# Optimization experiments

Hardware: AMD Instinct MI355X
Metric: run time of the kernel (lower is better)

The kernel has to match this reference:

```python
import jax, jax.numpy as jnp
import numpy as np

NUM_GROUPS = 32
NUM_HEADS = 4
EPS = 1e-5


def setup_inputs() -> dict:
    key = jax.random.key(0)
    ks = jax.random.split(key, 6)
    B, C, H, W = 16, 512, 32, 32
    x = jax.random.normal(ks[0], (B, C, H, W), dtype=jnp.float32)
    gn_w = jax.random.normal(ks[1], (C,), dtype=jnp.float32) * 0.02 + 1.0
    gn_b = jax.random.normal(ks[2], (C,), dtype=jnp.float32) * 0.02
    # 1x1 convs are channel matmuls: store as [out_ch, in_ch]
    w_qkv = jax.random.normal(ks[3], (3 * C, C), dtype=jnp.float32) * (C ** -0.5)
    w_out = jax.random.normal(ks[4], (C, C), dtype=jnp.float32) * (C ** -0.5)
    b_out = jax.random.normal(ks[5], (C,), dtype=jnp.float32) * 0.02
    return {"x": x, "gn_w": gn_w, "gn_b": gn_b, "w_qkv": w_qkv, "w_out": w_out, "b_out": b_out}


def _group_norm(x, w, b):
    B, C, H, W = x.shape
    g = NUM_GROUPS
    xg = x.reshape(B, g, C // g, H, W)
    mean = xg.mean(axis=(2, 3, 4), keepdims=True)
    var = xg.var(axis=(2, 3, 4), keepdims=True)
    xn = ((xg - mean) * jax.lax.rsqrt(var + EPS)).reshape(B, C, H, W)
    return xn * w[None, :, None, None] + b[None, :, None, None]


def reference(x, gn_w, gn_b, w_qkv, w_out, b_out):
    B, C, H, W = x.shape
    h = NUM_HEADS
    d = C // h
    scale = d ** -0.5
    xn = _group_norm(x, gn_w, gn_b)
    # 1x1 conv QKV projection: [3C, C] @ channels
    qkv = jnp.einsum('oc,bchw->bohw', w_qkv, xn)
    q, k, v = jnp.split(qkv, 3, axis=1)
    # [B, h, d, HW]
    q = q.reshape(B, h, d, H * W)
    k = k.reshape(B, h, d, H * W)
    v = v.reshape(B, h, d, H * W)
    scores = jnp.einsum('bhdi,bhdj->bhij', q, k) * scale
    probs = jax.nn.softmax(scores, axis=-1)
    out = jnp.einsum('bhij,bhdj->bhdi', probs, v)
    out = out.reshape(B, C, H, W)
    out = jnp.einsum('oc,bchw->bohw', w_out, out) + b_out[None, :, None, None]
    return out + x
```

## Files before the change

kernel.cpp:

```cpp
#include <hip/hip_runtime.h>
#include <hip/hip_bf16.h>

#define B_    16
#define C_    512
#define HW_   1024
#define G_    32
#define CPG_  16
#define NH_   4
#define D_    128
#define EPS_  1e-5f
#define SCALE_ 0.08838834764831845f
#define SCALE_L2E_ 0.1275174306f

typedef short bf16x8 __attribute__((ext_vector_type(8)));
typedef short bf16x4 __attribute__((ext_vector_type(4)));
typedef float f32x4  __attribute__((ext_vector_type(4)));

typedef __attribute__((address_space(3))) unsigned int lds_u32_t;
typedef const __attribute__((address_space(1))) unsigned int glb_u32_t;

__device__ __forceinline__ bf16x8 ld8(const __hip_bfloat16* p) {
    return *reinterpret_cast<const bf16x8*>(p);
}
__device__ __forceinline__ void gload16(const __hip_bfloat16* g, __hip_bfloat16* l) {
    __builtin_amdgcn_global_load_lds((glb_u32_t*)(const void*)g,
                                     (lds_u32_t*)(void*)l, 16, 0, 0);
}
__device__ __forceinline__ unsigned pack_bf2(float a, float b) {
    union { __hip_bfloat16 h; unsigned short u; } ua, ub;
    ua.h = __float2bfloat16(a); ub.h = __float2bfloat16(b);
    return ((unsigned)ub.u << 16) | (unsigned)ua.u;
}

__global__ __launch_bounds__(256) void convert_w(
    const float* __restrict__ wqkv, const float* __restrict__ wout,
    __hip_bfloat16* __restrict__ wqkv_bf, __hip_bfloat16* __restrict__ wout_bf) {
    const int i = (blockIdx.x * 256 + threadIdx.x) * 4;
    if (i < 3 * C_ * C_) {
        float4 v = *reinterpret_cast<const float4*>(wqkv + i);
        union { bf16x4 s; __hip_bfloat16 h[4]; } u;
        u.h[0] = __float2bfloat16(v.x); u.h[1] = __float2bfloat16(v.y);
        u.h[2] = __float2bfloat16(v.z); u.h[3] = __float2bfloat16(v.w);
        *reinterpret_cast<bf16x4*>(wqkv_bf + i) = u.s;
    }
    if (i < C_ * C_) {
        float4 v = *reinterpret_cast<const float4*>(wout + i);
        union { bf16x4 s; __hip_bfloat16 h[4]; } u;
        u.h[0] = __float2bfloat16(v.x); u.h[1] = __float2bfloat16(v.y);
        u.h[2] = __float2bfloat16(v.z); u.h[3] = __float2bfloat16(v.w);
        *reinterpret_cast<bf16x4*>(wout_bf + i) = u.s;
    }
}

__global__ __launch_bounds__(256) void gn_kernel(
    const float* __restrict__ x, const float* __restrict__ gnw,
    const float* __restrict__ gnb, __hip_bfloat16* __restrict__ xn_t) {
    const int b = blockIdx.x >> 5;
    const int g = blockIdx.x & 31;
    const float* xp = x + ((size_t)(b * C_ + g * CPG_)) * HW_;

    float s = 0.f, s2 = 0.f;
    const float4* xv = reinterpret_cast<const float4*>(xp);
    #pragma unroll
    for (int t = 0; t < 16; ++t) {
        float4 v = xv[threadIdx.x + t * 256];
        s  += v.x + v.y + v.z + v.w;
        s2 += v.x * v.x + v.y * v.y + v.z * v.z + v.w * v.w;
    }
    #pragma unroll
    for (int off = 32; off > 0; off >>= 1) {
        s  += __shfl_down(s,  off, 64);
        s2 += __shfl_down(s2, off, 64);
    }
    __shared__ float ss[4], ss2[4];
    if ((threadIdx.x & 63) == 0) { ss[threadIdx.x >> 6] = s; ss2[threadIdx.x >> 6] = s2; }
    __syncthreads();
    s = ss[0] + ss[1] + ss[2] + ss[3];
    s2 = ss2[0] + ss2[1] + ss2[2] + ss2[3];
    const float mean = s * (1.f / 16384.f);
    const float inv  = rsqrtf(fmaxf(s2 * (1.f / 16384.f) - mean * mean, 0.f) + EPS_);

    float a[16], bb[16];
    #pragma unroll
    for (int cc = 0; cc < 16; ++cc) {
        float w = gnw[g * CPG_ + cc];
        a[cc] = inv * w;
        bb[cc] = gnb[g * CPG_ + cc] - mean * inv * w;
    }

    for (int hw = threadIdx.x; hw < HW_; hw += 256) {
        union { bf16x8 v; __hip_bfloat16 h[8]; } u0, u1;
        #pragma unroll
        for (int cc = 0; cc < 8; ++cc)
            u0.h[cc] = __float2bfloat16(xp[cc * HW_ + hw] * a[cc] + bb[cc]);
        #pragma unroll
        for (int cc = 8; cc < 16; ++cc)
            u1.h[cc - 8] = __float2bfloat16(xp[cc * HW_ + hw] * a[cc] + bb[cc]);
        __hip_bfloat16* dst = xn_t + ((size_t)(b * HW_ + hw)) * C_ + g * CPG_;
        *reinterpret_cast<bf16x8*>(dst) = u0.v;
        *reinterpret_cast<bf16x8*>(dst + 8) = u1.v;
    }
}

#define PH_(r, s) (((r) * 8 + ((s) ^ ((r) & 7))) * 8)

__global__ __launch_bounds__(256, 3) void qkv_gemm(
    const __hip_bfloat16* __restrict__ W, const __hip_bfloat16* __restrict__ xn_t,
    __hip_bfloat16* __restrict__ q_t, __hip_bfloat16* __restrict__ k_t,
    __hip_bfloat16* __restrict__ v_s) {
    const int id   = blockIdx.x;
    const int virt = (id & 7) * 192 + (id >> 3);
    const int ot   = virt % 12;
    const int rest = virt / 12;
    const int itl  = rest & 7;
    const int b    = rest >> 3;
    const int o0 = ot * 128, i0 = itl * 128;

    const int t = threadIdx.x;
    const int w = t >> 6, lane = t & 63, l16 = lane & 15, lg = lane >> 4;
    const int wr = w >> 1, wc = w & 1;
    const __hip_bfloat16* xb = xn_t + (size_t)b * HW_ * C_;

    __shared__ __align__(16) __hip_bfloat16 Ab[128 * 64];
    __shared__ __align__(16) __hip_bfloat16 Bb[128 * 64];

    const int r8  = lane >> 3;
    const int ssl = (lane & 7) ^ r8;
    auto issue = [&](int kk) {
        #pragma unroll
        for (int j = 0; j < 4; ++j) {
            const int row = w * 32 + j * 8 + r8;
            gload16(W  + (size_t)(o0 + row) * C_ + kk + ssl * 8, &Ab[(w * 32 + j * 8) * 64]);
            gload16(xb + (size_t)(i0 + row) * C_ + kk + ssl * 8, &Bb[(w * 32 + j * 8) * 64]);
        }
    };

    f32x4 acc[4][4];
    const f32x4 z = {0.f, 0.f, 0.f, 0.f};
    #pragma unroll
    for (int m = 0; m < 4; ++m)
        #pragma unroll
        for (int n = 0; n < 4; ++n) acc[m][n] = z;

    for (int ks = 0; ks < 8; ++ks) {
        issue(ks * 64);
        __syncthreads();
        #pragma unroll
        for (int kks = 0; kks < 2; ++kks) {
            bf16x8 af[4], bfr[4];
            #pragma unroll
            for (int m = 0; m < 4; ++m)
                af[m] = ld8(&Ab[PH_(wr * 64 + m * 16 + l16, kks * 4 + lg)]);
            #pragma unroll
            for (int n = 0; n < 4; ++n)
                bfr[n] = ld8(&Bb[PH_(wc * 64 + n * 16 + l16, kks * 4 + lg)]);
            if (ot < 8) {
                #pragma unroll
                for (int m = 0; m < 4; ++m)
                    #pragma unroll
                    for (int n = 0; n < 4; ++n)
                        acc[m][n] = __builtin_amdgcn_mfma_f32_16x16x32_bf16(bfr[n], af[m], acc[m][n], 0, 0, 0);
            } else {
                #pragma unroll
                for (int m = 0; m < 4; ++m)
                    #pragma unroll
                    for (int n = 0; n < 4; ++n)
                        acc[m][n] = __builtin_amdgcn_mfma_f32_16x16x32_bf16(af[m], bfr[n], acc[m][n], 0, 0, 0);
            }
        }
        if (ks < 7) __syncthreads();
    }

    if (ot < 4) {
        const int hd = ot;
        __hip_bfloat16* base = q_t + (size_t)(b * NH_ + hd) * HW_ * D_;
        const int dd = wr * 64 + l16;
        #pragma unroll
        for (int m = 0; m < 4; ++m)
            #pragma unroll
            for (int n = 0; n < 4; ++n)
                #pragma unroll
                for (int r = 0; r < 4; ++r) {
                    const int i = i0 + wc * 64 + n * 16 + lg * 4 + r;
                    base[(size_t)i * D_ + dd + m * 16] = __float2bfloat16(acc[m][n][r] * SCALE_L2E_);
                }
    } else if (ot < 8) {
        const int hd = ot - 4;
        __hip_bfloat16* base = k_t + (size_t)(b * NH_ + hd) * HW_ * D_;
        const int dd = wr * 64 + l16;
        #pragma unroll
        for (int m = 0; m < 4; ++m)
            #pragma unroll
            for (int n = 0; n < 4; ++n)
                #pragma unroll
                for (int r = 0; r < 4; ++r) {
                    const int i = i0 + wc * 64 + n * 16 + lg * 4 + r;
                    base[(size_t)i * D_ + dd + m * 16] = __float2bfloat16(acc[m][n][r]);
                }
    } else {
        const int hd = ot - 8;
        __hip_bfloat16* base = v_s + (size_t)(b * NH_ + hd) * D_ * HW_;
        #pragma unroll
        for (int m = 0; m < 4; ++m)
            #pragma unroll
            for (int r = 0; r < 4; ++r) {
                const int dd = wr * 64 + m * 16 + lg * 4 + r;
                #pragma unroll
                for (int n = 0; n < 4; ++n) {
                    const int i = i0 + wc * 64 + n * 16 + l16;
                    base[(size_t)dd * HW_ + i] = __float2bfloat16(acc[m][n][r]);
                }
            }
    }
}

__global__ __launch_bounds__(512, 4) void attn_kernel(
    const __hip_bfloat16* __restrict__ q_t, const __hip_bfloat16* __restrict__ k_t,
    const __hip_bfloat16* __restrict__ v_s, __hip_bfloat16* __restrict__ at) {
    const int id  = blockIdx.x;
    const int xcd = id & 7;
    const int q8  = id >> 3;
    const int hb  = xcd * 8 + (q8 >> 3);
    const int it  = q8 & 7;
    const int h   = hb & 3;
    const int b   = hb >> 2;

    const int t = threadIdx.x;
    const int w  = t >> 6;
    const int lane = t & 63;
    const int l16 = lane & 15, lg = lane >> 4;
    const size_t bh = (size_t)b * NH_ + h;
    const __hip_bfloat16* qp = q_t + bh * HW_ * D_;
    const __hip_bfloat16* kp = k_t + bh * HW_ * D_;
    const __hip_bfloat16* vp = v_s + bh * D_ * HW_;
    const int i0 = it * 128 + w * 16;

    __shared__ __align__(16) __hip_bfloat16 kbuf[64 * 128];
    __shared__ __align__(16) __hip_bfloat16 vbuf[128 * 64];
    __shared__ __align__(16) __hip_bfloat16 P2[8][16][72];

    #define KPHYS(row, c) (((row) * 16 + ((c) ^ ((row) & 7))) * 8)
    #define VPHYS(row, c) (((row) * 8  + ((c) ^ ((row) & 7))) * 8)

    const int krow = t >> 3, kc = t & 7;
    const int vrow = t >> 2, vc = t & 3;

    bf16x8 kreg0, kreg1, vreg0, vreg1;
    auto issue_loads = [&](int j0) {
        kreg0 = ld8(kp + (size_t)(j0 + krow) * D_ + kc * 8);
        kreg1 = ld8(kp + (size_t)(j0 + krow) * D_ + (kc + 8) * 8);
        vreg0 = ld8(vp + (size_t)vrow * HW_ + j0 + vc * 8);
        vreg1 = ld8(vp + (size_t)vrow * HW_ + j0 + (vc + 4) * 8);
    };

    bf16x8 aq[4];
    #pragma unroll
    for (int kd = 0; kd < 4; ++kd)
        aq[kd] = ld8(qp + (size_t)(i0 + l16) * D_ + kd * 32 + lg * 8);

    f32x4 accO[8];
    const f32x4 z = {0.f, 0.f, 0.f, 0.f};
    #pragma unroll
    for (int tt = 0; tt < 8; ++tt) accO[tt] = z;
    float m_run = -INFINITY;
    float l_run = 0.f;

    issue_loads(0);

    for (int jb = 0; jb < 16; ++jb) {
        __syncthreads();
        *reinterpret_cast<bf16x8*>(&kbuf[KPHYS(krow, kc)])     = kreg0;
        *reinterpret_cast<bf16x8*>(&kbuf[KPHYS(krow, kc + 8)]) = kreg1;
        *reinterpret_cast<bf16x8*>(&vbuf[VPHYS(vrow, vc)])     = vreg0;
        *reinterpret_cast<bf16x8*>(&vbuf[VPHYS(vrow, vc + 4)]) = vreg1;
        __syncthreads();
        if (jb < 15) issue_loads((jb + 1) * 64);

        f32x4 st[4];
        #pragma unroll
        for (int jt = 0; jt < 4; ++jt) st[jt] = z;
        #pragma unroll
        for (int jt = 0; jt < 4; ++jt)
            #pragma unroll
            for (int kd = 0; kd < 4; ++kd) {
                bf16x8 bk = ld8(&kbuf[KPHYS(jt * 16 + l16, kd * 4 + lg)]);
                st[jt] = __builtin_amdgcn_mfma_f32_16x16x32_bf16(bk, aq[kd], st[jt], 0, 0, 0);
            }

        float mx = fmaxf(fmaxf(st[0][0], st[0][1]), fmaxf(st[0][2], st[0][3]));
        #pragma unroll
        for (int jt = 1; jt < 4; ++jt)
            mx = fmaxf(mx, fmaxf(fmaxf(st[jt][0], st[jt][1]), fmaxf(st[jt][2], st[jt][3])));
        mx = fmaxf(mx, __shfl_xor(mx, 16, 64));
        mx = fmaxf(mx, __shfl_xor(mx, 32, 64));

        if (__any(mx > m_run + 8.f)) {
            float mnew = fmaxf(m_run, mx);
            float alpha = exp2f(m_run - mnew);
            m_run = mnew;
            l_run *= alpha;
            float al[4];
            #pragma unroll
            for (int r = 0; r < 4; ++r) al[r] = __shfl(alpha, lg * 4 + r, 64);
            const f32x4 a4 = {al[0], al[1], al[2], al[3]};
            #pragma unroll
            for (int tt = 0; tt < 8; ++tt) accO[tt] *= a4;
        }

        float sum = 0.f;
        #pragma unroll
        for (int jt = 0; jt < 4; ++jt) {
            float p0 = exp2f(st[jt][0] - m_run), p1 = exp2f(st[jt][1] - m_run);
            float p2 = exp2f(st[jt][2] - m_run), p3 = exp2f(st[jt][3] - m_run);
            sum += (p0 + p1) + (p2 + p3);
            uint2 uu = { pack_bf2(p0, p1), pack_bf2(p2, p3) };
            *reinterpret_cast<uint2*>(&P2[w][l16][jt * 16 + lg * 4]) = uu;
        }
        sum += __shfl_xor(sum, 16, 64);
        sum += __shfl_xor(sum, 32, 64);
        l_run += sum;

        #pragma unroll
        for (int ks = 0; ks < 2; ++ks) {
            bf16x8 pa = ld8(&P2[w][l16][ks * 32 + lg * 8]);
            #pragma unroll
            for (int dt = 0; dt < 8; ++dt) {
                bf16x8 bv = ld8(&vbuf[VPHYS(dt * 16 + l16, ks * 4 + lg)]);
                accO[dt] = __builtin_amdgcn_mfma_f32_16x16x32_bf16(pa, bv, accO[dt], 0, 0, 0);
            }
        }
    }

    const float linv = 1.f / l_run;
    float rl[4];
    #pragma unroll
    for (int r = 0; r < 4; ++r) rl[r] = __shfl(linv, lg * 4 + r, 64);
    #pragma unroll
    for (int r = 0; r < 4; ++r) {
        const int i = i0 + lg * 4 + r;
        #pragma unroll
        for (int dt = 0; dt < 8; ++dt)
            at[((size_t)b * HW_ + i) * C_ + h * D_ + dt * 16 + l16] =
                __float2bfloat16(accO[dt][r] * rl[r]);
    }
    #undef KPHYS
    #undef VPHYS
}

__global__ __launch_bounds__(256, 3) void out_gemm(
    const __hip_bfloat16* __restrict__ W, const __hip_bfloat16* __restrict__ at,
    const float* __restrict__ b_out, const float* __restrict__ x,
    float* __restrict__ out) {
    const int id   = blockIdx.x;
    const int virt = (id & 7) * 64 + (id >> 3);
    const int ot   = virt & 3;
    const int rest = virt >> 2;
    const int itl  = rest & 7;
    const int b    = rest >> 3;
    const int o0 = ot * 128, i0 = itl * 128;

    const int t = threadIdx.x;
    const int w = t >> 6, lane = t & 63, l16 = lane & 15, lg = lane >> 4;
    const int wr = w >> 1, wc = w & 1;
    const __hip_bfloat16* ab = at + (size_t)b * HW_ * C_;

    __shared__ __align__(16) __hip_bfloat16 Ab[128 * 64];
    __shared__ __align__(16) __hip_bfloat16 Bb[128 * 64];

    const int r8  = lane >> 3;
    const int ssl = (lane & 7) ^ r8;
    auto issue = [&](int kk) {
        #pragma unroll
        for (int j = 0; j < 4; ++j) {
            const int row = w * 32 + j * 8 + r8;
            gload16(W  + (size_t)(o0 + row) * C_ + kk + ssl * 8, &Ab[(w * 32 + j * 8) * 64]);
            gload16(ab + (size_t)(i0 + row) * C_ + kk + ssl * 8, &Bb[(w * 32 + j * 8) * 64]);
        }
    };

    f32x4 acc[4][4];
    const f32x4 z = {0.f, 0.f, 0.f, 0.f};
    #pragma unroll
    for (int m = 0; m < 4; ++m)
        #pragma unroll
        for (int n = 0; n < 4; ++n) acc[m][n] = z;

    for (int ks = 0; ks < 8; ++ks) {
        issue(ks * 64);
        __syncthreads();
        #pragma unroll
        for (int kks = 0; kks < 2; ++kks) {
            bf16x8 af[4], bfr[4];
            #pragma unroll
            for (int m = 0; m < 4; ++m)
                af[m] = ld8(&Ab[PH_(wr * 64 + m * 16 + l16, kks * 4 + lg)]);
            #pragma unroll
            for (int n = 0; n < 4; ++n)
                bfr[n] = ld8(&Bb[PH_(wc * 64 + n * 16 + l16, kks * 4 + lg)]);
            #pragma unroll
            for (int m = 0; m < 4; ++m)
                #pragma unroll
                for (int n = 0; n < 4; ++n)
                    acc[m][n] = __builtin_amdgcn_mfma_f32_16x16x32_bf16(af[m], bfr[n], acc[m][n], 0, 0, 0);
        }
        if (ks < 7) __syncthreads();
    }

    #pragma unroll
    for (int m = 0; m < 4; ++m)
        #pragma unroll
        for (int r = 0; r < 4; ++r) {
            const int o = o0 + wr * 64 + m * 16 + lg * 4 + r;
            const float bo = b_out[o];
            #pragma unroll
            for (int n = 0; n < 4; ++n) {
                const int i = i0 + wc * 64 + n * 16 + l16;
                const size_t idx = ((size_t)(b * C_ + o)) * HW_ + i;
                out[idx] = acc[m][n][r] + bo + x[idx];
            }
        }
}

extern "C" void kernel_launch(void* const* d_in, const int* in_sizes, int n_in,
                              void* d_out, int out_size, void* d_ws, size_t ws_size,
                              hipStream_t stream) {
    (void)in_sizes; (void)n_in; (void)out_size; (void)ws_size;
    const float* x     = (const float*)d_in[0];
    const float* gn_w  = (const float*)d_in[1];
    const float* gn_b  = (const float*)d_in[2];
    const float* w_qkv = (const float*)d_in[3];
    const float* w_out = (const float*)d_in[4];
    const float* b_out = (const float*)d_in[5];
    float* out = (float*)d_out;

    char* ws = (char*)d_ws;
    size_t off = 0;
    auto alloc = [&](size_t bytes) { void* p = ws + off; off += (bytes + 255) & ~255ULL; return p; };
    __hip_bfloat16* wqkv_bf = (__hip_bfloat16*)alloc((size_t)3 * C_ * C_ * 2);
    __hip_bfloat16* wout_bf = (__hip_bfloat16*)alloc((size_t)C_ * C_ * 2);
    __hip_bfloat16* xn_t    = (__hip_bfloat16*)alloc((size_t)B_ * HW_ * C_ * 2);
    __hip_bfloat16* q_t     = (__hip_bfloat16*)alloc((size_t)B_ * HW_ * C_ * 2);
    __hip_bfloat16* k_t     = (__hip_bfloat16*)alloc((size_t)B_ * HW_ * C_ * 2);
    __hip_bfloat16* v_s     = (__hip_bfloat16*)alloc((size_t)B_ * HW_ * C_ * 2);
    __hip_bfloat16* at      = xn_t;

    convert_w<<<768, 256, 0, stream>>>(w_qkv, w_out, wqkv_bf, wout_bf);
    gn_kernel<<<512, 256, 0, stream>>>(x, gn_w, gn_b, xn_t);
    qkv_gemm<<<1536, 256, 0, stream>>>(wqkv_bf, xn_t, q_t, k_t, v_s);
    attn_kernel<<<512, 512, 0, stream>>>(q_t, k_t, v_s, at);
    out_gemm<<<512, 256, 0, stream>>>(wout_bf, at, b_out, x, out);
}
```

Measured before the change: 154.0 us.

## Double-buffer LDS tiles in QKV and output projection GEMMs

Both projection GEMMs now keep two LDS buffers per operand. The next K-slice's global-to-LDS loads are issued right after the barrier, so they overlap the MFMA work on the current slice, and the loop drops to one barrier per iteration. This hides global load latency at the cost of doubling LDS use to 64 KB per block, and launch bounds drop from 3 to 2 blocks per CU. Correctness depends on the async gload16 completing before the next barrier; how it waits is not visible here.

```diff
diff --git a/kernel.cpp b/kernel.cpp
--- a/kernel.cpp
+++ b/kernel.cpp
@@ -104,7 +104,7 @@
 
 #define PH_(r, s) (((r) * 8 + ((s) ^ ((r) & 7))) * 8)
 
-__global__ __launch_bounds__(256, 3) void qkv_gemm(
+__global__ __launch_bounds__(256, 2) void qkv_gemm(
     const __hip_bfloat16* __restrict__ W, const __hip_bfloat16* __restrict__ xn_t,
     __hip_bfloat16* __restrict__ q_t, __hip_bfloat16* __restrict__ k_t,
     __hip_bfloat16* __restrict__ v_s) {
@@ -121,17 +121,17 @@
     const int wr = w >> 1, wc = w & 1;
     const __hip_bfloat16* xb = xn_t + (size_t)b * HW_ * C_;
 
-    __shared__ __align__(16) __hip_bfloat16 Ab[128 * 64];
-    __shared__ __align__(16) __hip_bfloat16 Bb[128 * 64];
+    __shared__ __align__(16) __hip_bfloat16 Ab[2][128 * 64];
+    __shared__ __align__(16) __hip_bfloat16 Bb[2][128 * 64];
 
     const int r8  = lane >> 3;
     const int ssl = (lane & 7) ^ r8;
-    auto issue = [&](int kk) {
+    auto issue = [&](int kk, int bi) {
         #pragma unroll
         for (int j = 0; j < 4; ++j) {
             const int row = w * 32 + j * 8 + r8;
-            gload16(W  + (size_t)(o0 + row) * C_ + kk + ssl * 8, &Ab[(w * 32 + j * 8) * 64]);
-            gload16(xb + (size_t)(i0 + row) * C_ + kk + ssl * 8, &Bb[(w * 32 + j * 8) * 64]);
+            gload16(W  + (size_t)(o0 + row) * C_ + kk + ssl * 8, &Ab[bi][(w * 32 + j * 8) * 64]);
+            gload16(xb + (size_t)(i0 + row) * C_ + kk + ssl * 8, &Bb[bi][(w * 32 + j * 8) * 64]);
         }
     };
 
@@ -142,18 +142,21 @@
         #pragma unroll
         for (int n = 0; n < 4; ++n) acc[m][n] = z;
 
+    issue(0, 0);
     for (int ks = 0; ks < 8; ++ks) {
-        issue(ks * 64);
         __syncthreads();
+        if (ks < 7) issue((ks + 1) * 64, (ks + 1) & 1);
+        const __hip_bfloat16* Ac = Ab[ks & 1];
+        const __hip_bfloat16* Bc = Bb[ks & 1];
         #pragma unroll
         for (int kks = 0; kks < 2; ++kks) {
             bf16x8 af[4], bfr[4];
             #pragma unroll
             for (int m = 0; m < 4; ++m)
-                af[m] = ld8(&Ab[PH_(wr * 64 + m * 16 + l16, kks * 4 + lg)]);
+                af[m] = ld8(&Ac[PH_(wr * 64 + m * 16 + l16, kks * 4 + lg)]);
             #pragma unroll
             for (int n = 0; n < 4; ++n)
-                bfr[n] = ld8(&Bb[PH_(wc * 64 + n * 16 + l16, kks * 4 + lg)]);
+                bfr[n] = ld8(&Bc[PH_(wc * 64 + n * 16 + l16, kks * 4 + lg)]);
             if (ot < 8) {
                 #pragma unroll
                 for (int m = 0; m < 4; ++m)
@@ -168,7 +171,6 @@
                         acc[m][n] = __builtin_amdgcn_mfma_f32_16x16x32_bf16(af[m], bfr[n], acc[m][n], 0, 0, 0);
             }
         }
-        if (ks < 7) __syncthreads();
     }
 
     if (ot < 4) {
@@ -347,7 +349,7 @@
     #undef VPHYS
 }
 
-__global__ __launch_bounds__(256, 3) void out_gemm(
+__global__ __launch_bounds__(256, 2) void out_gemm(
     const __hip_bfloat16* __restrict__ W, const __hip_bfloat16* __restrict__ at,
     const float* __restrict__ b_out, const float* __restrict__ x,
     float* __restrict__ out) {
@@ -364,17 +366,17 @@
     const int wr = w >> 1, wc = w & 1;
     const __hip_bfloat16* ab = at + (size_t)b * HW_ * C_;
 
-    __shared__ __align__(16) __hip_bfloat16 Ab[128 * 64];
-    __shared__ __align__(16) __hip_bfloat16 Bb[128 * 64];
+    __shared__ __align__(16) __hip_bfloat16 Ab[2][128 * 64];
+    __shared__ __align__(16) __hip_bfloat16 Bb[2][128 * 64];
 
     const int r8  = lane >> 3;
     const int ssl = (lane & 7) ^ r8;
-    auto issue = [&](int kk) {
+    auto issue = [&](int kk, int bi) {
         #pragma unroll
         for (int j = 0; j < 4; ++j) {
             const int row = w * 32 + j * 8 + r8;
-            gload16(W  + (size_t)(o0 + row) * C_ + kk + ssl * 8, &Ab[(w * 32 + j * 8) * 64]);
-            gload16(ab + (size_t)(i0 + row) * C_ + kk + ssl * 8, &Bb[(w * 32 + j * 8) * 64]);
+            gload16(W  + (size_t)(o0 + row) * C_ + kk + ssl * 8, &Ab[bi][(w * 32 + j * 8) * 64]);
+            gload16(ab + (size_t)(i0 + row) * C_ + kk + ssl * 8, &Bb[bi][(w * 32 + j * 8) * 64]);
         }
     };
 
@@ -385,25 +387,27 @@
         #pragma unroll
         for (int n = 0; n < 4; ++n) acc[m][n] = z;
 
+    issue(0, 0);
     for (int ks = 0; ks < 8; ++ks) {
-        issue(ks * 64);
         __syncthreads();
+        if (ks < 7) issue((ks + 1) * 64, (ks + 1) & 1);
+        const __hip_bfloat16* Ac = Ab[ks & 1];
+        const __hip_bfloat16* Bc = Bb[ks & 1];
         #pragma unroll
         for (int kks = 0; kks < 2; ++kks) {
             bf16x8 af[4], bfr[4];
             #pragma unroll
             for (int m = 0; m < 4; ++m)
-                af[m] = ld8(&Ab[PH_(wr * 64 + m * 16 + l16, kks * 4 + lg)]);
+                af[m] = ld8(&Ac[PH_(wr * 64 + m * 16 + l16, kks * 4 + lg)]);
             #pragma unroll
             for (int n = 0; n < 4; ++n)
-                bfr[n] = ld8(&Bb[PH_(wc * 64 + n * 16 + l16, kks * 4 + lg)]);
+                bfr[n] = ld8(&Bc[PH_(wc * 64 + n * 16 + l16, kks * 4 + lg)]);
             #pragma unroll
             for (int m = 0; m < 4; ++m)
                 #pragma unroll
                 for (int n = 0; n < 4; ++n)
                     acc[m][n] = __builtin_amdgcn_mfma_f32_16x16x32_bf16(af[m], bfr[n], acc[m][n], 0, 0, 0);
         }
-        if (ks < 7) __syncthreads();
     }
 
     #pragma unroll
```

Measured after the change: 130.4 us. 1.18x faster.
